# Kernel optimization log

Hardware: AMD Instinct MI355X
Metric: run time of the kernel (lower is better)

The kernel has to match this reference:

```python
import jax, jax.numpy as jnp
import numpy as np

N = 50000      # nodes
E = 800000     # edges
F_IN = 256
HID = [256, 256, 512]
G = 512        # graphs
FP = 2048      # fingerprint size


def setup_inputs() -> dict:
    key = jax.random.key(0)
    ks = jax.random.split(key, 14)
    node_features = jax.random.normal(ks[0], (N, F_IN), dtype=jnp.float32)
    edge_index = jax.random.randint(ks[1], (2, E), 0, N, dtype=jnp.int64)
    batch = jnp.sort(jax.random.randint(ks[2], (N,), 0, G, dtype=jnp.int64))

    def lin(k, fi, fo):
        s = 1.0 / np.sqrt(fi)
        kw, kb = jax.random.split(k)
        W = jax.random.uniform(kw, (fi, fo), jnp.float32, -s, s)
        b = jax.random.uniform(kb, (fo,), jnp.float32, -s, s)
        return W, b

    W1, b1 = lin(ks[3], F_IN, HID[0])
    W2, b2 = lin(ks[4], HID[0], HID[1])
    W3, b3 = lin(ks[5], HID[1], HID[2])
    pw, pb = lin(ks[6], HID[2], 1)          # PoolWeightedSum gating linear
    Wo, bo = lin(ks[7], 2 * HID[2], FP)     # head: weight_sum + max concat
    return dict(node_features=node_features, edge_index=edge_index, batch=batch,
                W1=W1, b1=b1, W2=W2, b2=b2, W3=W3, b3=b3,
                pw=pw, pb=pb, Wo=Wo, bo=bo)


def _gcn_layer(x, src, dst, W, b):
    # GCNConv: add self-loops, symmetric normalization, h = x @ W, aggregate.
    n = x.shape[0]
    h = x @ W  # [N, F_out]
    loop = jnp.arange(n, dtype=src.dtype)
    s = jnp.concatenate([src, loop])
    d = jnp.concatenate([dst, loop])
    deg = jax.ops.segment_sum(jnp.ones(s.shape[0], h.dtype), d, num_segments=n)
    dis = jax.lax.rsqrt(deg)  # deg >= 1 because of self-loops
    norm = dis[s] * dis[d]    # [E+N]
    out = jax.ops.segment_sum(h[s] * norm[:, None], d, num_segments=n)
    return out + b


def _forward(node_features, edge_index, batch,
             W1, b1, W2, b2, W3, b3, pw, pb, Wo, bo):
    src, dst = edge_index[0], edge_index[1]
    x = node_features
    for W, b in ((W1, b1), (W2, b2), (W3, b3)):
        x = jax.nn.relu(_gcn_layer(x, src, dst, W, b))

    # PoolWeightedSum: sigmoid-gated node features, scatter-add per graph
    w = jax.nn.sigmoid(x @ pw + pb)  # [N, 1]
    pooled_ws = jax.ops.segment_sum(x * w, batch, num_segments=G,
                                    indices_are_sorted=True)
    # PoolMax: scatter-max per graph (empty segments -> 0, like torch zeros init)
    pooled_max = jax.ops.segment_max(x, batch, num_segments=G,
                                     indices_are_sorted=True)
    pooled_max = jnp.where(jnp.isfinite(pooled_max), pooled_max, 0.0)

    feats = jnp.concatenate([pooled_ws, pooled_max], axis=1)  # [G, 2*HID[-1]]
    return jax.nn.relu(feats @ Wo + bo)  # [G, FP]


def reference(node_features, edge_index, batch,
              W1, b1, W2, b2, W3, b3, pw, pb, Wo, bo):
    return _forward(node_features, edge_index, batch,
                    W1, b1, W2, b2, W3, b3, pw, pb, Wo, bo)
```

## Files before the change

### kernel.cpp

```cpp
#include <hip/hip_runtime.h>
#include <math.h>

#define NNODES 50000
#define NEDGES 800000
#define NGRAPH 512
#define FIN    256
#define H1     256
#define H2     256
#define H3     512
#define FPOUT  2048

typedef __attribute__((ext_vector_type(8))) short short8;
typedef __attribute__((ext_vector_type(8))) _Float16 half8;
typedef __attribute__((ext_vector_type(4))) float floatx4;
typedef __attribute__((ext_vector_type(4))) unsigned short ushx4;

__device__ inline float h2f(ushort u) { return (float)__builtin_bit_cast(_Float16, u); }
__device__ inline ushort f2h(float x) { return __builtin_bit_cast(ushort, (_Float16)x); }
__device__ inline void split2h(float a, ushort& h, ushort& l) {
    _Float16 hh = (_Float16)a;
    h = __builtin_bit_cast(ushort, hh);
    l = f2h(a - (float)hh);
}


__global__ __launch_bounds__(256) void zero_i32(int* p, int n) {
    int i = blockIdx.x * 256 + threadIdx.x;
    if (i < n) p[i] = 0;
}

__global__ __launch_bounds__(256) void count_deg(const int* __restrict__ ei, int* __restrict__ degi, int e_total) {
    int e = blockIdx.x * 256 + threadIdx.x;
    if (e >= e_total) return;
    int d = ei[e_total + e];
    atomicAdd(&degi[d], 1);
}

__global__ __launch_bounds__(256) void calc_dis(const int* __restrict__ degi, float* __restrict__ dis, int n) {
    int i = blockIdx.x * 256 + threadIdx.x;
    if (i < n) dis[i] = rsqrtf((float)(degi[i] + 1));
}

__global__ __launch_bounds__(256) void scanA(const int* __restrict__ degi, int* __restrict__ offs,
                                             int* __restrict__ partials, int n) {
    __shared__ int sm[256];
    int t = threadIdx.x, idx = blockIdx.x * 256 + t;
    int v = (idx < n) ? degi[idx] : 0;
    sm[t] = v; __syncthreads();
    for (int d = 1; d < 256; d <<= 1) {
        int add = (t >= d) ? sm[t - d] : 0;
        __syncthreads();
        sm[t] += add;
        __syncthreads();
    }
    if (idx < n) offs[idx + 1] = sm[t];
    if (t == 255) partials[blockIdx.x] = sm[255];
}

__global__ __launch_bounds__(256) void scanB(int* __restrict__ partials, int nb) {
    __shared__ int sm[256];
    int t = threadIdx.x;
    int v = (t < nb) ? partials[t] : 0;
    sm[t] = v; __syncthreads();
    for (int d = 1; d < 256; d <<= 1) {
        int add = (t >= d) ? sm[t - d] : 0;
        __syncthreads();
        sm[t] += add;
        __syncthreads();
    }
    if (t < nb) partials[t] = sm[t] - v;
}

__global__ __launch_bounds__(256) void scanC(int* __restrict__ offs, const int* __restrict__ partials, int n) {
    int idx = blockIdx.x * 256 + threadIdx.x;
    if (idx < n) offs[idx + 1] += partials[blockIdx.x];
    if (idx == 0) offs[0] = 0;
}

__global__ __launch_bounds__(256) void copy_i32(const int* __restrict__ a, int* __restrict__ b, int n) {
    int i = blockIdx.x * 256 + threadIdx.x;
    if (i < n) b[i] = a[i];
}

__global__ __launch_bounds__(256) void fill_csr(const int* __restrict__ ei, const float* __restrict__ dis,
                                                int* __restrict__ curs, int* __restrict__ csr_src,
                                                float* __restrict__ csr_w, int e_total) {
    int e = blockIdx.x * 256 + threadIdx.x;
    if (e >= e_total) return;
    int s = ei[e];
    int d = ei[e_total + e];
    int pos = atomicAdd(&curs[d], 1);
    csr_src[pos] = s;
    csr_w[pos] = dis[s] * dis[d];
}

__global__ __launch_bounds__(256) void wsplit_t(const float* __restrict__ W, ushort* __restrict__ hi,
                                                ushort* __restrict__ lo, int K, int N) {
    __shared__ float sm[32][33];
    int tx = threadIdx.x & 31, ty = threadIdx.x >> 5;
    int n0 = blockIdx.x * 32, k0 = blockIdx.y * 32;
    #pragma unroll
    for (int j = 0; j < 32; j += 8)
        sm[ty + j][tx] = W[(size_t)(k0 + ty + j) * N + n0 + tx];
    __syncthreads();
    #pragma unroll
    for (int j = 0; j < 32; j += 8) {
        float a = sm[tx][ty + j];
        ushort h, l; split2h(a, h, l);
        size_t o = (size_t)(n0 + ty + j) * K + k0 + tx;
        hi[o] = h; lo[o] = l;
    }
}

__global__ __launch_bounds__(256) void conv_f16(const float* __restrict__ x, ushort* __restrict__ xh, int total4) {
    int i = blockIdx.x * 256 + threadIdx.x;
    if (i >= total4) return;
    float4 a = ((const float4*)x)[i];
    ushx4 h = {f2h(a.x), f2h(a.y), f2h(a.z), f2h(a.w)};
    ((ushx4*)xh)[i] = h;
}

#define LSTR 40
template<int SPLIT>
__global__ __launch_bounds__(256) void gemm_f16(const ushort* __restrict__ Ahp, const ushort* __restrict__ Alp,
                                                const ushort* __restrict__ Bhp, const ushort* __restrict__ Blp,
                                                float* __restrict__ C, ushort* __restrict__ Ch,
                                                const float* __restrict__ bias,
                                                int M, int N, int K, int do_relu, int outmode) {
    __shared__ _Float16 lsA[128 * LSTR];
    __shared__ _Float16 lsB[128 * LSTR];
    __shared__ _Float16 lsAl[SPLIT ? 128 * LSTR : 8];
    __shared__ _Float16 lsBl[SPLIT ? 128 * LSTR : 8];
    const _Float16* Ah = (const _Float16*)Ahp;
    const _Float16* Al = (const _Float16*)Alp;
    const _Float16* Bh = (const _Float16*)Bhp;
    const _Float16* Bl = (const _Float16*)Blp;

    int tid = threadIdx.x;
    int w = tid >> 6, lane = tid & 63;
    int quad = lane >> 4, lr = lane & 15;
    int wm = w & 1, wn = w >> 1;
    int row0 = blockIdx.y * 128, col0 = blockIdx.x * 128;

    floatx4 acc[4][4];
    #pragma unroll
    for (int i = 0; i < 4; ++i)
        #pragma unroll
        for (int j = 0; j < 4; ++j)
            acc[i][j] = (floatx4){0.f, 0.f, 0.f, 0.f};

    const half8 zer = {};
    int srow = tid >> 2;
    int skk  = (tid & 3) * 8;

    half8 pa[2], pb[2], pal[2], pbl[2];
    #pragma unroll
    for (int c = 0; c < 2; ++c) {
        int row = c * 64 + srow;
        bool mok = (row0 + row) < M;
        size_t aoff = (size_t)(row0 + row) * K + skk;
        pa[c] = mok ? *(const half8*)(Ah + aoff) : zer;
        if constexpr (SPLIT) pal[c] = mok ? *(const half8*)(Al + aoff) : zer;
        size_t boff = (size_t)(col0 + row) * K + skk;
        pb[c] = *(const half8*)(Bh + boff);
        if constexpr (SPLIT) pbl[c] = *(const half8*)(Bl + boff);
    }

    for (int k0 = 0; k0 < K; k0 += 32) {
        #pragma unroll
        for (int c = 0; c < 2; ++c) {
            int lo = (c * 64 + srow) * LSTR + skk;
            *(half8*)(lsA + lo) = pa[c];
            *(half8*)(lsB + lo) = pb[c];
            if constexpr (SPLIT) { *(half8*)(lsAl + lo) = pal[c]; *(half8*)(lsBl + lo) = pbl[c]; }
        }
        __syncthreads();
        if (k0 + 32 < K) {
            #pragma unroll
            for (int c = 0; c < 2; ++c) {
                int row = c * 64 + srow;
                bool mok = (row0 + row) < M;
                size_t aoff = (size_t)(row0 + row) * K + k0 + 32 + skk;
                pa[c] = mok ? *(const half8*)(Ah + aoff) : zer;
                if constexpr (SPLIT) pal[c] = mok ? *(const half8*)(Al + aoff) : zer;
                size_t boff = (size_t)(col0 + row) * K + k0 + 32 + skk;
                pb[c] = *(const half8*)(Bh + boff);
                if constexpr (SPLIT) pbl[c] = *(const half8*)(Bl + boff);
            }
        }
        half8 af[4], afl[4];
        #pragma unroll
        for (int mt = 0; mt < 4; ++mt) {
            int ao = (wm * 64 + mt * 16 + lr) * LSTR + quad * 8;
            af[mt] = *(const half8*)(lsA + ao);
            if constexpr (SPLIT) afl[mt] = *(const half8*)(lsAl + ao);
        }
        #pragma unroll
        for (int nt = 0; nt < 4; ++nt) {
            int bo = (wn * 64 + nt * 16 + lr) * LSTR + quad * 8;
            half8 bf = *(const half8*)(lsB + bo);
            half8 bfl;
            if constexpr (SPLIT) bfl = *(const half8*)(lsBl + bo);
            #pragma unroll
            for (int mt = 0; mt < 4; ++mt) {
                acc[mt][nt] = __builtin_amdgcn_mfma_f32_16x16x32_f16(af[mt], bf, acc[mt][nt], 0, 0, 0);
                if constexpr (SPLIT) {
                    acc[mt][nt] = __builtin_amdgcn_mfma_f32_16x16x32_f16(af[mt], bfl, acc[mt][nt], 0, 0, 0);
                    acc[mt][nt] = __builtin_amdgcn_mfma_f32_16x16x32_f16(afl[mt], bf, acc[mt][nt], 0, 0, 0);
                }
            }
        }
        __syncthreads();
    }

    #pragma unroll
    for (int mt = 0; mt < 4; ++mt) {
        #pragma unroll
        for (int r = 0; r < 4; ++r) {
            int row = row0 + wm * 64 + mt * 16 + quad * 4 + r;
            if (row >= M) continue;
            #pragma unroll
            for (int nt = 0; nt < 4; ++nt) {
                int col = col0 + wn * 64 + nt * 16 + lr;
                float v = acc[mt][nt][r] + bias[col];
                if (do_relu) v = v > 0.f ? v : 0.f;
                if (outmode) Ch[(size_t)row * N + col] = f2h(v);
                else         C[(size_t)row * N + col] = v;
            }
        }
    }
}

__global__ __launch_bounds__(256) void agg256b(const ushort* __restrict__ xh, ushort* __restrict__ yh,
                                               const float* __restrict__ dis,
                                               const int* __restrict__ offs, const int* __restrict__ csr_src,
                                               const float* __restrict__ csr_w) {
    constexpr int F = 256;
    int wave = threadIdx.x >> 6;
    int lane = threadIdx.x & 63;
    int half = lane >> 5;
    int sub  = lane & 31;
    int v = blockIdx.x * 8 + wave * 2 + half;
    int beg = offs[v], end = offs[v + 1];
    int len = end - beg;
    int leno = __shfl_xor(len, 32, 64);
    int maxlen = len > leno ? len : leno;

    float dv = dis[v];
    float sw = dv * dv;
    short8 a0 = ((const short8*)(xh + (size_t)v * F))[sub];
    float acc[8];
    #pragma unroll
    for (int j = 0; j < 8; ++j) acc[j] = h2f((ushort)a0[j]) * sw;

    for (int k = 0; k < maxlen; k += 8) {
        int   s[8];
        float w[8];
        #pragma unroll
        for (int u = 0; u < 8; ++u) {
            int idx = beg + k + u;
            bool val = idx < end;
            int ic = val ? idx : 0;
            s[u] = csr_src[ic];
            w[u] = val ? csr_w[ic] : 0.f;
        }
        short8 g[8];
        #pragma unroll
        for (int u = 0; u < 8; ++u)
            g[u] = ((const short8*)(xh + (size_t)s[u] * F))[sub];
        #pragma unroll
        for (int u = 0; u < 8; ++u) {
            #pragma unroll
            for (int j = 0; j < 8; ++j)
                acc[j] += h2f((ushort)g[u][j]) * w[u];
        }
    }

    ushort h[8];
    #pragma unroll
    for (int j = 0; j < 8; ++j) h[j] = f2h(acc[j]);
    short8 hv = {(short)h[0], (short)h[1], (short)h[2], (short)h[3], (short)h[4], (short)h[5], (short)h[6], (short)h[7]};
    ((short8*)(yh + (size_t)v * F))[sub] = hv;
}

__global__ __launch_bounds__(256) void gatepool(const float* __restrict__ x, const float* __restrict__ pw,
                                                const float* __restrict__ pb, const int* __restrict__ batch,
                                                ushort* __restrict__ phi, ushort* __restrict__ plo, int n) {
    int g = blockIdx.x;
    int t = threadIdx.x;
    int wave = t >> 6, lane = t & 63;
    int lo_ = 0, hi_ = n;
    while (lo_ < hi_) { int mid = (lo_ + hi_) >> 1; if (batch[mid] < g) lo_ = mid + 1; else hi_ = mid; }
    int start = lo_;
    hi_ = n;
    while (lo_ < hi_) { int mid = (lo_ + hi_) >> 1; if (batch[mid] < g + 1) lo_ = mid + 1; else hi_ = mid; }
    int end = lo_;

    const float4* pwv = (const float4*)pw;
    float4 wa = pwv[lane], wb = pwv[lane + 64];
    float pb0 = pb[0];

    float4 s0 = make_float4(0.f, 0.f, 0.f, 0.f), s1 = s0;
    float4 m0 = make_float4(-INFINITY, -INFINITY, -INFINITY, -INFINITY), m1 = m0;

    for (int nn = start + wave; nn < end; nn += 4) {
        const float4* xr = (const float4*)(x + (size_t)nn * 512);
        float4 a = xr[lane];
        float4 b = xr[lane + 64];
        float p = a.x * wa.x + a.y * wa.y + a.z * wa.z + a.w * wa.w
                + b.x * wb.x + b.y * wb.y + b.z * wb.z + b.w * wb.w;
        #pragma unroll
        for (int off = 32; off; off >>= 1) p += __shfl_down(p, off, 64);
        float wg = __shfl(p, 0, 64);
        wg = 1.f / (1.f + expf(-(wg + pb0)));
        s0.x += a.x * wg; s0.y += a.y * wg; s0.z += a.z * wg; s0.w += a.w * wg;
        s1.x += b.x * wg; s1.y += b.y * wg; s1.z += b.z * wg; s1.w += b.w * wg;
        m0.x = fmaxf(m0.x, a.x); m0.y = fmaxf(m0.y, a.y); m0.z = fmaxf(m0.z, a.z); m0.w = fmaxf(m0.w, a.w);
        m1.x = fmaxf(m1.x, b.x); m1.y = fmaxf(m1.y, b.y); m1.z = fmaxf(m1.z, b.z); m1.w = fmaxf(m1.w, b.w);
    }

    __shared__ float ls[4][1024];
    *(float4*)&ls[wave][lane * 4]       = s0;
    *(float4*)&ls[wave][256 + lane * 4] = s1;
    *(float4*)&ls[wave][512 + lane * 4] = m0;
    *(float4*)&ls[wave][768 + lane * 4] = m1;
    __syncthreads();

    float sa = ls[0][t] + ls[1][t] + ls[2][t] + ls[3][t];
    float sb = ls[0][t + 256] + ls[1][t + 256] + ls[2][t + 256] + ls[3][t + 256];
    float ma = fmaxf(fmaxf(ls[0][512 + t], ls[1][512 + t]), fmaxf(ls[2][512 + t], ls[3][512 + t]));
    float mb = fmaxf(fmaxf(ls[0][768 + t], ls[1][768 + t]), fmaxf(ls[2][768 + t], ls[3][768 + t]));
    if (start >= end) { ma = 0.f; mb = 0.f; }
    ushort h, l;
    size_t base = (size_t)g * 1024;
    split2h(sa, h, l); phi[base + t] = h;       plo[base + t] = l;
    split2h(sb, h, l); phi[base + 256 + t] = h; plo[base + 256 + t] = l;
    split2h(ma, h, l); phi[base + 512 + t] = h; plo[base + 512 + t] = l;
    split2h(mb, h, l); phi[base + 768 + t] = h; plo[base + 768 + t] = l;
}


extern "C" void kernel_launch(void* const* d_in, const int* in_sizes, int n_in,
                              void* d_out, int out_size, void* d_ws, size_t ws_size,
                              hipStream_t stream) {
    const float* x0    = (const float*)d_in[0];
    const int*   ei    = (const int*)d_in[1];
    const int*   batch = (const int*)d_in[2];
    const float* W1 = (const float*)d_in[3];
    const float* b1 = (const float*)d_in[4];
    const float* W2 = (const float*)d_in[5];
    const float* b2 = (const float*)d_in[6];
    const float* W3 = (const float*)d_in[7];
    const float* b3 = (const float*)d_in[8];
    const float* pw = (const float*)d_in[9];
    const float* pb = (const float*)d_in[10];
    const float* Wo = (const float*)d_in[11];
    const float* bo = (const float*)d_in[12];
    float* out = (float*)d_out;

    float* ws = (float*)d_ws;
    size_t off = 0;
    float* bufB = ws + off; off += (size_t)NNODES * 512;
    ushort* xh  = (ushort*)(ws + off); off += (size_t)NNODES * 256 / 2;
    ushort* yh  = (ushort*)(ws + off); off += (size_t)NNODES * 256 / 2;
    ushort* ylo_unused = (ushort*)(ws + off); off += (size_t)NNODES * 256 / 2;
    (void)ylo_unused;
    ushort* W1thi = (ushort*)(ws + off); off += 256 * 256 / 2;
    ushort* W1tlo = (ushort*)(ws + off); off += 256 * 256 / 2;
    ushort* W2thi = (ushort*)(ws + off); off += 256 * 256 / 2;
    ushort* W2tlo = (ushort*)(ws + off); off += 256 * 256 / 2;
    ushort* W3thi = (ushort*)(ws + off); off += 512 * 256 / 2;
    ushort* W3tlo = (ushort*)(ws + off); off += 512 * 256 / 2;
    ushort* Wothi = (ushort*)(ws + off); off += (size_t)FPOUT * 1024 / 2;
    ushort* Wotlo = (ushort*)(ws + off); off += (size_t)FPOUT * 1024 / 2;
    ushort* phi = (ushort*)(ws + off); off += (size_t)NGRAPH * 1024 / 2;
    ushort* plo = (ushort*)(ws + off); off += (size_t)NGRAPH * 1024 / 2;
    float* dis  = ws + off; off += NNODES;
    int*   degi = (int*)(ws + off); off += NNODES;
    int*   offs = (int*)(ws + off); off += (NNODES + 4);
    int*   curs = (int*)(ws + off); off += NNODES;
    int*   csr_src = (int*)(ws + off); off += NEDGES;
    float* csr_w   = ws + off; off += NEDGES;
    int*   partials = (int*)(ws + off); off += 256;

    const int NB_N = (NNODES + 255) / 256;
    const int NB_E = (NEDGES + 255) / 256;
    const int NB_A = NNODES / 8;
    const int MB128 = (NNODES + 127) / 128;

    { dim3 g(256 / 32, 256 / 32);    wsplit_t<<<g, 256, 0, stream>>>(W1, W1thi, W1tlo, 256, 256); }
    { dim3 g(256 / 32, 256 / 32);    wsplit_t<<<g, 256, 0, stream>>>(W2, W2thi, W2tlo, 256, 256); }
    { dim3 g(512 / 32, 256 / 32);    wsplit_t<<<g, 256, 0, stream>>>(W3, W3thi, W3tlo, 256, 512); }
    { dim3 g(FPOUT / 32, 1024 / 32); wsplit_t<<<g, 256, 0, stream>>>(Wo, Wothi, Wotlo, 1024, FPOUT); }

    zero_i32<<<NB_N, 256, 0, stream>>>(degi, NNODES);
    count_deg<<<NB_E, 256, 0, stream>>>(ei, degi, NEDGES);
    calc_dis<<<NB_N, 256, 0, stream>>>(degi, dis, NNODES);
    scanA<<<NB_N, 256, 0, stream>>>(degi, offs, partials, NNODES);
    scanB<<<1, 256, 0, stream>>>(partials, NB_N);
    scanC<<<NB_N, 256, 0, stream>>>(offs, partials, NNODES);
    copy_i32<<<NB_N, 256, 0, stream>>>(offs, curs, NNODES);
    fill_csr<<<NB_E, 256, 0, stream>>>(ei, dis, curs, csr_src, csr_w, NEDGES);

    conv_f16<<<(NNODES * 256 / 4 + 255) / 256, 256, 0, stream>>>(x0, xh, NNODES * 256 / 4);

    agg256b<<<NB_A, 256, 0, stream>>>(xh, yh, dis, offs, csr_src, csr_w);
    {
        dim3 grid(H1 / 128, MB128);
        gemm_f16<0><<<grid, 256, 0, stream>>>(yh, nullptr, W1thi, nullptr, nullptr, xh, b1, NNODES, H1, FIN, 1, 1);
    }
    agg256b<<<NB_A, 256, 0, stream>>>(xh, yh, dis, offs, csr_src, csr_w);
    {
        dim3 grid(H2 / 128, MB128);
        gemm_f16<0><<<grid, 256, 0, stream>>>(yh, nullptr, W2thi, nullptr, nullptr, xh, b2, NNODES, H2, H1, 1, 1);
    }
    agg256b<<<NB_A, 256, 0, stream>>>(xh, yh, dis, offs, csr_src, csr_w);
    {
        dim3 grid(H3 / 128, MB128);
        gemm_f16<0><<<grid, 256, 0, stream>>>(yh, nullptr, W3thi, nullptr, bufB, nullptr, b3, NNODES, H3, H2, 1, 0);
    }
    gatepool<<<NGRAPH, 256, 0, stream>>>(bufB, pw, pb, batch, phi, plo, NNODES);
    {
        dim3 grid(FPOUT / 128, (NGRAPH + 127) / 128);
        gemm_f16<1><<<grid, 256, 0, stream>>>(phi, plo, Wothi, Wotlo, out, nullptr, bo, NGRAPH, FPOUT, 1024, 1, 0);
    }
}
```

Measured before the change: 605.3 us.

## Split-K the head GEMM, pack CSR pairs, and build CSR from atomic ranks

The head GEMM (512x2048x1024) ran on only 64 blocks. It now uses a 4-way split-K grid that writes partial sums to scratch, and a new head_fin kernel reduces them and adds bias and ReLU. CSR construction records each edge's atomic rank during degree counting, so fill_csr computes positions without a second atomic pass or the copy kernel. The source index and edge weight are packed into one int2, so aggregation does a single 8-byte load per edge. The cost is extra partial-sum traffic and one more kernel launch.

```diff
diff --git a/kernel.cpp b/kernel.cpp
--- a/kernel.cpp
+++ b/kernel.cpp
@@ -29,11 +29,12 @@
     if (i < n) p[i] = 0;
 }
 
-__global__ __launch_bounds__(256) void count_deg(const int* __restrict__ ei, int* __restrict__ degi, int e_total) {
+__global__ __launch_bounds__(256) void count_deg(const int* __restrict__ ei, int* __restrict__ degi,
+                                                 int* __restrict__ rank, int e_total) {
     int e = blockIdx.x * 256 + threadIdx.x;
     if (e >= e_total) return;
     int d = ei[e_total + e];
-    atomicAdd(&degi[d], 1);
+    rank[e] = atomicAdd(&degi[d], 1);
 }
 
 __global__ __launch_bounds__(256) void calc_dis(const int* __restrict__ degi, float* __restrict__ dis, int n) {
@@ -77,21 +78,18 @@
     if (idx == 0) offs[0] = 0;
 }
 
-__global__ __launch_bounds__(256) void copy_i32(const int* __restrict__ a, int* __restrict__ b, int n) {
-    int i = blockIdx.x * 256 + threadIdx.x;
-    if (i < n) b[i] = a[i];
-}
-
 __global__ __launch_bounds__(256) void fill_csr(const int* __restrict__ ei, const float* __restrict__ dis,
-                                                int* __restrict__ curs, int* __restrict__ csr_src,
-                                                float* __restrict__ csr_w, int e_total) {
+                                                const int* __restrict__ offs, const int* __restrict__ rank,
+                                                int2* __restrict__ csr_pair, int e_total) {
     int e = blockIdx.x * 256 + threadIdx.x;
     if (e >= e_total) return;
     int s = ei[e];
     int d = ei[e_total + e];
-    int pos = atomicAdd(&curs[d], 1);
-    csr_src[pos] = s;
-    csr_w[pos] = dis[s] * dis[d];
+    int pos = offs[d] + rank[e];
+    int2 pr;
+    pr.x = s;
+    pr.y = __float_as_int(dis[s] * dis[d]);
+    csr_pair[pos] = pr;
 }
 
 __global__ __launch_bounds__(256) void wsplit_t(const float* __restrict__ W, ushort* __restrict__ hi,
@@ -126,7 +124,8 @@
                                                 const ushort* __restrict__ Bhp, const ushort* __restrict__ Blp,
                                                 float* __restrict__ C, ushort* __restrict__ Ch,
                                                 const float* __restrict__ bias,
-                                                int M, int N, int K, int do_relu, int outmode) {
+                                                int M, int N, int K, int do_relu, int outmode,
+                                                int kspan, int accmode) {
     __shared__ _Float16 lsA[128 * LSTR];
     __shared__ _Float16 lsB[128 * LSTR];
     __shared__ _Float16 lsAl[SPLIT ? 128 * LSTR : 8];
@@ -141,6 +140,7 @@
     int quad = lane >> 4, lr = lane & 15;
     int wm = w & 1, wn = w >> 1;
     int row0 = blockIdx.y * 128, col0 = blockIdx.x * 128;
+    int kb = blockIdx.z * kspan;
 
     floatx4 acc[4][4];
     #pragma unroll
@@ -158,15 +158,15 @@
     for (int c = 0; c < 2; ++c) {
         int row = c * 64 + srow;
         bool mok = (row0 + row) < M;
-        size_t aoff = (size_t)(row0 + row) * K + skk;
+        size_t aoff = (size_t)(row0 + row) * K + kb + skk;
         pa[c] = mok ? *(const half8*)(Ah + aoff) : zer;
         if constexpr (SPLIT) pal[c] = mok ? *(const half8*)(Al + aoff) : zer;
-        size_t boff = (size_t)(col0 + row) * K + skk;
+        size_t boff = (size_t)(col0 + row) * K + kb + skk;
         pb[c] = *(const half8*)(Bh + boff);
         if constexpr (SPLIT) pbl[c] = *(const half8*)(Bl + boff);
     }
 
-    for (int k0 = 0; k0 < K; k0 += 32) {
+    for (int k0 = kb; k0 < kb + kspan; k0 += 32) {
         #pragma unroll
         for (int c = 0; c < 2; ++c) {
             int lo = (c * 64 + srow) * LSTR + skk;
@@ -175,7 +175,7 @@
             if constexpr (SPLIT) { *(half8*)(lsAl + lo) = pal[c]; *(half8*)(lsBl + lo) = pbl[c]; }
         }
         __syncthreads();
-        if (k0 + 32 < K) {
+        if (k0 + 32 < kb + kspan) {
             #pragma unroll
             for (int c = 0; c < 2; ++c) {
                 int row = c * 64 + srow;
@@ -213,6 +213,7 @@
         __syncthreads();
     }
 
+    size_t zoff = accmode ? (size_t)blockIdx.z * M * N : 0;
     #pragma unroll
     for (int mt = 0; mt < 4; ++mt) {
         #pragma unroll
@@ -222,19 +223,42 @@
             #pragma unroll
             for (int nt = 0; nt < 4; ++nt) {
                 int col = col0 + wn * 64 + nt * 16 + lr;
-                float v = acc[mt][nt][r] + bias[col];
-                if (do_relu) v = v > 0.f ? v : 0.f;
+                float v = acc[mt][nt][r];
+                if (!accmode) {
+                    v += bias[col];
+                    if (do_relu) v = v > 0.f ? v : 0.f;
+                }
                 if (outmode) Ch[(size_t)row * N + col] = f2h(v);
-                else         C[(size_t)row * N + col] = v;
+                else         C[zoff + (size_t)row * N + col] = v;
             }
         }
     }
+}
+
+__global__ __launch_bounds__(256) void head_fin(const float* __restrict__ part, const float* __restrict__ bo,
+                                                float* __restrict__ out) {
+    int i4 = blockIdx.x * 256 + threadIdx.x;
+    const int TOT4 = NGRAPH * FPOUT / 4;
+    if (i4 >= TOT4) return;
+    int col4 = i4 & (FPOUT / 4 - 1);
+    const size_t STRIDE4 = (size_t)NGRAPH * FPOUT / 4;
+    const float4* p = (const float4*)part;
+    float4 a = p[i4];
+    float4 b = p[i4 + STRIDE4];
+    float4 c = p[i4 + 2 * STRIDE4];
+    float4 d = p[i4 + 3 * STRIDE4];
+    float4 bb = ((const float4*)bo)[col4];
+    float4 o;
+    o.x = a.x + b.x + c.x + d.x + bb.x; o.x = o.x > 0.f ? o.x : 0.f;
+    o.y = a.y + b.y + c.y + d.y + bb.y; o.y = o.y > 0.f ? o.y : 0.f;
+    o.z = a.z + b.z + c.z + d.z + bb.z; o.z = o.z > 0.f ? o.z : 0.f;
+    o.w = a.w + b.w + c.w + d.w + bb.w; o.w = o.w > 0.f ? o.w : 0.f;
+    ((float4*)out)[i4] = o;
 }
 
 __global__ __launch_bounds__(256) void agg256b(const ushort* __restrict__ xh, ushort* __restrict__ yh,
                                                const float* __restrict__ dis,
-                                               const int* __restrict__ offs, const int* __restrict__ csr_src,
-                                               const float* __restrict__ csr_w) {
+                                               const int* __restrict__ offs, const int2* __restrict__ csr_pair) {
     constexpr int F = 256;
     int wave = threadIdx.x >> 6;
     int lane = threadIdx.x & 63;
@@ -260,9 +284,10 @@
         for (int u = 0; u < 8; ++u) {
             int idx = beg + k + u;
             bool val = idx < end;
-            int ic = val ? idx : 0;
-            s[u] = csr_src[ic];
-            w[u] = val ? csr_w[ic] : 0.f;
+            int ic = val ? idx : beg;
+            int2 pr = csr_pair[ic];
+            s[u] = pr.x;
+            w[u] = val ? __int_as_float(pr.y) : 0.f;
         }
         short8 g[8];
         #pragma unroll
@@ -363,8 +388,7 @@
     float* bufB = ws + off; off += (size_t)NNODES * 512;
     ushort* xh  = (ushort*)(ws + off); off += (size_t)NNODES * 256 / 2;
     ushort* yh  = (ushort*)(ws + off); off += (size_t)NNODES * 256 / 2;
-    ushort* ylo_unused = (ushort*)(ws + off); off += (size_t)NNODES * 256 / 2;
-    (void)ylo_unused;
+    int*    rank = (int*)(ws + off);   off += (size_t)NNODES * 256 / 2;
     ushort* W1thi = (ushort*)(ws + off); off += 256 * 256 / 2;
     ushort* W1tlo = (ushort*)(ws + off); off += 256 * 256 / 2;
     ushort* W2thi = (ushort*)(ws + off); off += 256 * 256 / 2;
@@ -378,9 +402,9 @@
     float* dis  = ws + off; off += NNODES;
     int*   degi = (int*)(ws + off); off += NNODES;
     int*   offs = (int*)(ws + off); off += (NNODES + 4);
-    int*   curs = (int*)(ws + off); off += NNODES;
-    int*   csr_src = (int*)(ws + off); off += NEDGES;
-    float* csr_w   = ws + off; off += NEDGES;
+    int*   curs_unused = (int*)(ws + off); off += NNODES;
+    (void)curs_unused;
+    int2*  csr_pair = (int2*)(ws + off); off += 2 * (size_t)NEDGES;
     int*   partials = (int*)(ws + off); off += 256;
 
     const int NB_N = (NNODES + 255) / 256;
@@ -394,34 +418,38 @@
     { dim3 g(FPOUT / 32, 1024 / 32); wsplit_t<<<g, 256, 0, stream>>>(Wo, Wothi, Wotlo, 1024, FPOUT); }
 
     zero_i32<<<NB_N, 256, 0, stream>>>(degi, NNODES);
-    count_deg<<<NB_E, 256, 0, stream>>>(ei, degi, NEDGES);
+    count_deg<<<NB_E, 256, 0, stream>>>(ei, degi, rank, NEDGES);
     calc_dis<<<NB_N, 256, 0, stream>>>(degi, dis, NNODES);
     scanA<<<NB_N, 256, 0, stream>>>(degi, offs, partials, NNODES);
     scanB<<<1, 256, 0, stream>>>(partials, NB_N);
     scanC<<<NB_N, 256, 0, stream>>>(offs, partials, NNODES);
-    copy_i32<<<NB_N, 256, 0, stream>>>(offs, curs, NNODES);
-    fill_csr<<<NB_E, 256, 0, stream>>>(ei, dis, curs, csr_src, csr_w, NEDGES);
+    fill_csr<<<NB_E, 256, 0, stream>>>(ei, dis, offs, rank, csr_pair, NEDGES);
 
     conv_f16<<<(NNODES * 256 / 4 + 255) / 256, 256, 0, stream>>>(x0, xh, NNODES * 256 / 4);
 
-    agg256b<<<NB_A, 256, 0, stream>>>(xh, yh, dis, offs, csr_src, csr_w);
+    agg256b<<<NB_A, 256, 0, stream>>>(xh, yh, dis, offs, csr_pair);
     {
         dim3 grid(H1 / 128, MB128);
-        gemm_f16<0><<<grid, 256, 0, stream>>>(yh, nullptr, W1thi, nullptr, nullptr, xh, b1, NNODES, H1, FIN, 1, 1);
-    }
-    agg256b<<<NB_A, 256, 0, stream>>>(xh, yh, dis, offs, csr_src, csr_w);
+        gemm_f16<0><<<grid, 256, 0, stream>>>(yh, nullptr, W1thi, nullptr, nullptr, xh, b1,
+                                              NNODES, H1, FIN, 1, 1, FIN, 0);
+    }
+    agg256b<<<NB_A, 256, 0, stream>>>(xh, yh, dis, offs, csr_pair);
     {
         dim3 grid(H2 / 128, MB128);
-        gemm_f16<0><<<grid, 256, 0, stream>>>(yh, nullptr, W2thi, nullptr, nullptr, xh, b2, NNODES, H2, H1, 1, 1);
-    }
-    agg256b<<<NB_A, 256, 0, stream>>>(xh, yh, dis, offs, csr_src, csr_w);
+        gemm_f16<0><<<grid, 256, 0, stream>>>(yh, nullptr, W2thi, nullptr, nullptr, xh, b2,
+                                              NNODES, H2, H1, 1, 1, H1, 0);
+    }
+    agg256b<<<NB_A, 256, 0, stream>>>(xh, yh, dis, offs, csr_pair);
     {
         dim3 grid(H3 / 128, MB128);
-        gemm_f16<0><<<grid, 256, 0, stream>>>(yh, nullptr, W3thi, nullptr, bufB, nullptr, b3, NNODES, H3, H2, 1, 0);
+        gemm_f16<0><<<grid, 256, 0, stream>>>(yh, nullptr, W3thi, nullptr, bufB, nullptr, b3,
+                                              NNODES, H3, H2, 1, 0, H2, 0);
     }
     gatepool<<<NGRAPH, 256, 0, stream>>>(bufB, pw, pb, batch, phi, plo, NNODES);
     {
-        dim3 grid(FPOUT / 128, (NGRAPH + 127) / 128);
-        gemm_f16<1><<<grid, 256, 0, stream>>>(phi, plo, Wothi, Wotlo, out, nullptr, bo, NGRAPH, FPOUT, 1024, 1, 0);
-    }
-}
+        dim3 grid(FPOUT / 128, (NGRAPH + 127) / 128, 4);
+        gemm_f16<1><<<grid, 256, 0, stream>>>(phi, plo, Wothi, Wotlo, bufB, nullptr, nullptr,
+                                              NGRAPH, FPOUT, 1024, 0, 0, 256, 1);
+    }
+    head_fin<<<(NGRAPH * FPOUT / 4 + 255) / 256, 256, 0, stream>>>(bufB, bo, out);
+}
```

Measured after the change: 566.2 us. 1.07x faster.
